# Performance work log

Hardware: AMD Instinct MI355X
Metric: run time of the kernel (lower is better)

## Reference

```python
import jax, jax.numpy as jnp
import numpy as np

B, T, C, H = 8, 2048, 1024, 64  # batch, seq (block_size), n_embd, head_size


def setup_inputs() -> dict:
    key = jax.random.key(0)
    kx, kq, kk, kv = jax.random.split(key, 4)
    s = 1.0 / np.sqrt(C)
    return {
        "x": jax.random.normal(kx, (B, T, C), dtype=jnp.float32),
        "Wq": jax.random.normal(kq, (C, H), dtype=jnp.float32) * s,
        "Wk": jax.random.normal(kk, (C, H), dtype=jnp.float32) * s,
        "Wv": jax.random.normal(kv, (C, H), dtype=jnp.float32) * s,
    }


def reference(x, Wq, Wk, Wv):
    t = x.shape[1]
    q = jnp.einsum("btc,ch->bth", x, Wq)
    k = jnp.einsum("btc,ch->bth", x, Wk)
    v = jnp.einsum("btc,ch->bth", x, Wv)
    scores = jnp.einsum("bqh,bkh->bqk", q, k) / jnp.sqrt(jnp.float32(H))
    causal = jnp.tril(jnp.ones((t, t), dtype=bool))  # tril mask
    scores = jnp.where(causal, scores, -jnp.inf)
    attn = jax.nn.softmax(scores, axis=-1)
    return jnp.einsum("bqk,bkh->bqh", attn, v)
```

## Files before the change

### kernel.cpp

```cpp
#include <hip/hip_runtime.h>
#include <hip/hip_bf16.h>

#define BB 8
#define TT 2048
#define CC 1024
#define HH 64
#define NSPLIT 8

typedef __attribute__((ext_vector_type(8)))  short bf16x8;
typedef __attribute__((ext_vector_type(4)))  float f32x4;
typedef __attribute__((ext_vector_type(16))) float f32x16;
typedef __attribute__((ext_vector_type(8)))  unsigned short us8;
typedef unsigned int u32;

static __device__ __forceinline__ unsigned short f2bf(float f) {
    union { float f; unsigned int u; } v; v.f = f;
    unsigned int u = v.u;
    return (unsigned short)((u + 0x7FFFu + ((u >> 16) & 1u)) >> 16);
}
static __device__ __forceinline__ float bf2f(unsigned short s) {
    union { u32 u; float f; } v; v.u = ((u32)s) << 16; return v.f;
}

__global__ __launch_bounds__(256) void prep_weights(
        const float* __restrict__ Wq, const float* __restrict__ Wk,
        const float* __restrict__ Wv, unsigned short* __restrict__ Wt) {
    __shared__ float tile[64][65];
    int w  = blockIdx.x >> 4;
    int c0 = (blockIdx.x & 15) * 64;
    const float* W = (w == 0) ? Wq : (w == 1) ? Wk : Wv;
    int li = threadIdx.x;
    {
        int c = li >> 2, h4 = (li & 3) * 16;
        const float* src = W + (size_t)(c0 + c) * HH + h4;
        #pragma unroll
        for (int i = 0; i < 4; ++i) {
            float4 v4 = *(const float4*)(src + i * 4);
            tile[c][h4 + i*4 + 0] = v4.x; tile[c][h4 + i*4 + 1] = v4.y;
            tile[c][h4 + i*4 + 2] = v4.z; tile[c][h4 + i*4 + 3] = v4.w;
        }
    }
    __syncthreads();
    float scale = (w == 0) ? 0.1803368802f : 1.0f;
    int h = li >> 2, cg = (li & 3) * 16;
    unsigned short* dst = Wt + (size_t)w * HH * CC + (size_t)h * CC + c0 + cg;
    #pragma unroll
    for (int i = 0; i < 16; ++i) dst[i] = f2bf(tile[cg + i][h] * scale);
}

__global__ __launch_bounds__(512, 4) void proj_qkv(
        const float* __restrict__ x, const unsigned short* __restrict__ Wt,
        unsigned short* __restrict__ Pp) {
    __shared__ unsigned short Xs[2][64 * 64];
    __shared__ unsigned short Ws[2][192 * 64];
    int tid = threadIdx.x;
    int wv = tid >> 6, lane = tid & 63;
    int quad = (lane >> 4) & 3, lq = lane & 15;
    int mg = wv >> 2, ng = wv & 3;
    int r0 = blockIdx.x * 64;
    int k0 = blockIdx.y * 512;

    int xr = tid >> 3, xg = tid & 7;
    const float* xsrc = x + (size_t)(r0 + xr) * CC + k0 + xg * 8;
    int xdst = xr * 64 + ((xg ^ (xr & 7)) * 8);
    float4 xa[2], xb[2];

    f32x4 acc[2][3];
    #pragma unroll
    for (int mt = 0; mt < 2; ++mt)
        #pragma unroll
        for (int nt = 0; nt < 3; ++nt)
            #pragma unroll
            for (int i = 0; i < 4; ++i) acc[mt][nt][i] = 0.0f;

    auto stageW = [&](int buf, int kc) {
        #pragma unroll
        for (int i = 0; i < 3; ++i) {
            int fp = tid + i * 512;
            int r = fp >> 3, pb = fp & 7, g = pb ^ (r & 7);
            const u32 __attribute__((address_space(1)))* gsrc =
                (const u32 __attribute__((address_space(1)))*)
                    (Wt + (size_t)r * CC + k0 + kc * 64 + g * 8);
            u32 __attribute__((address_space(3)))* ldst =
                (u32 __attribute__((address_space(3)))*)(&Ws[buf][fp * 8]);
            __builtin_amdgcn_global_load_lds(gsrc, ldst, 16, 0, 0);
        }
    };
    auto loadX = [&](int set, int kc) {
        xa[set] = *(const float4*)(xsrc + kc * 64);
        xb[set] = *(const float4*)(xsrc + kc * 64 + 4);
    };
    auto writeX = [&](int set, int buf) {
        unsigned short h[8];
        h[0]=f2bf(xa[set].x); h[1]=f2bf(xa[set].y);
        h[2]=f2bf(xa[set].z); h[3]=f2bf(xa[set].w);
        h[4]=f2bf(xb[set].x); h[5]=f2bf(xb[set].y);
        h[6]=f2bf(xb[set].z); h[7]=f2bf(xb[set].w);
        *(us8*)&Xs[buf][xdst] = *(const us8*)h;
    };

    loadX(0, 0); loadX(1, 1);
    stageW(0, 0);
    writeX(0, 0);

    for (int kc = 0; kc < 8; ++kc) {
        int cur = kc & 1;
        __syncthreads();
        if (kc < 7) stageW(1 - cur, kc + 1);
        if (kc < 6) loadX(kc & 1, kc + 2);
        #pragma unroll
        for (int ks = 0; ks < 2; ++ks) {
            int g = ks * 4 + quad;
            bf16x8 a[2], b[3];
            #pragma unroll
            for (int mt = 0; mt < 2; ++mt) {
                int arow = mg * 32 + mt * 16 + lq;
                a[mt] = *(const bf16x8*)&Xs[cur][arow * 64 + (g ^ (lq & 7)) * 8];
            }
            #pragma unroll
            for (int nt = 0; nt < 3; ++nt) {
                int brow = ng * 48 + nt * 16 + lq;
                b[nt] = *(const bf16x8*)&Ws[cur][brow * 64 + (g ^ (lq & 7)) * 8];
            }
            #pragma unroll
            for (int mt = 0; mt < 2; ++mt)
                #pragma unroll
                for (int nt = 0; nt < 3; ++nt)
                    acc[mt][nt] = __builtin_amdgcn_mfma_f32_16x16x32_bf16(
                        a[mt], b[nt], acc[mt][nt], 0, 0, 0);
        }
        if (kc < 7) writeX((kc + 1) & 1, 1 - cur);
    }

    unsigned short* Pb =
        Pp + ((size_t)blockIdx.y * (BB * TT) + r0) * 192;
    #pragma unroll
    for (int mt = 0; mt < 2; ++mt) {
        #pragma unroll
        for (int nt = 0; nt < 3; ++nt) {
            int g = ng * 48 + nt * 16 + lq;
            #pragma unroll
            for (int i = 0; i < 4; ++i) {
                int row = mg * 32 + mt * 16 + quad * 4 + i;
                Pb[(size_t)row * 192 + g] = f2bf(acc[mt][nt][i]);
            }
        }
    }
}

__global__ __launch_bounds__(256) void qkv_reduce(
        const unsigned short* __restrict__ Pp,
        unsigned short* __restrict__ qws, unsigned short* __restrict__ kws,
        unsigned short* __restrict__ vws) {
    __shared__ unsigned short Vt[64][72];
    int t = threadIdx.x;
    int br0 = blockIdx.x * 64;
    const size_t H2 = (size_t)BB * TT * 192;
    {
        int r = br0 + (t >> 2), cg = (t & 3) * 32;
        const unsigned short* p0 = Pp + (size_t)r * 192 + cg;
        const unsigned short* p1 = p0 + H2;
        unsigned short* dst = (cg < 64) ? (qws + (size_t)r * HH + cg)
                                        : (kws + (size_t)r * HH + (cg - 64));
        #pragma unroll
        for (int u = 0; u < 4; ++u) {
            us8 a = *(const us8*)(p0 + u * 8);
            us8 b = *(const us8*)(p1 + u * 8);
            unsigned short o[8];
            #pragma unroll
            for (int j = 0; j < 8; ++j) o[j] = f2bf(bf2f(a[j]) + bf2f(b[j]));
            *(us8*)(dst + u * 8) = *(const us8*)o;
        }
    }
    {
        int r = br0 + (t >> 2), ch = (t & 3) * 16;
        const unsigned short* p0 = Pp + (size_t)r * 192 + 128 + ch;
        const unsigned short* p1 = p0 + H2;
        #pragma unroll
        for (int u = 0; u < 2; ++u) {
            us8 a = *(const us8*)(p0 + u * 8);
            us8 b = *(const us8*)(p1 + u * 8);
            #pragma unroll
            for (int j = 0; j < 8; ++j)
                Vt[ch + u * 8 + j][r & 63] = f2bf(bf2f(a[j]) + bf2f(b[j]));
        }
    }
    __syncthreads();
    {
        int h = t >> 2, tb = (t & 3) * 16;
        int b = br0 >> 11, rr = br0 & (TT - 1);
        #pragma unroll
        for (int u = 0; u < 2; ++u)
            *(us8*)(vws + ((size_t)b * HH + h) * TT + rr + tb + u * 8) =
                *(const us8*)&Vt[h][tb + u * 8];
    }
}

__global__ __launch_bounds__(128, 3) void attn(
        const unsigned short* __restrict__ qws,
        const unsigned short* __restrict__ kws,
        const unsigned short* __restrict__ vws,
        unsigned short* __restrict__ Op, float* __restrict__ Lp) {
    __shared__ unsigned short Kt[32][72];
    __shared__ unsigned short Vt[64][40];
    __shared__ unsigned short Ps[64][40];
    int ti = blockIdx.x;
    int s  = blockIdx.y;
    int b  = blockIdx.z;
    int last = 2 * ti + 1;
    if (s > last) return;
    int tid = threadIdx.x, wv = tid >> 6, lane = tid & 63;
    int half = lane >> 5, l31 = lane & 31;

    bf16x8 qf[4];
    {
        const unsigned short* qp =
            qws + ((size_t)b * TT + ti * 64 + wv * 32 + l31) * HH + half * 8;
        #pragma unroll
        for (int ks = 0; ks < 4; ++ks) qf[ks] = *(const bf16x8*)(qp + ks * 16);
    }
    f32x16 O0, O1, Lc;
    #pragma unroll
    for (int i = 0; i < 16; ++i) { O0[i] = 0.f; O1[i] = 0.f; Lc[i] = 0.f; }
    bf16x8 ones;
    #pragma unroll
    for (int i = 0; i < 8; ++i) ones[i] = (short)0x3F80;

    int kr = tid >> 3, kg = tid & 7;
    int vh = tid >> 2, vkb = tid & 3;
    const unsigned short* ksrc0 = kws + ((size_t)b * TT + kr) * HH + kg * 8;
    const unsigned short* vsrc0 = vws + ((size_t)b * HH + vh) * TT + vkb * 8;

    us8 rk[2], rv[2];
    auto loadKV = [&](int jc) {
        rk[0] = *(const us8*)(ksrc0 + (size_t)(jc * 32) * HH);
        rk[1] = *(const us8*)(ksrc0 + (size_t)(jc * 32 + 16) * HH);
        rv[0] = *(const us8*)(vsrc0 + jc * 32);
        rv[1] = *(const us8*)(vsrc0 + (size_t)32 * TT + jc * 32);
    };
    auto writeKV = [&]() {
        *(us8*)&Kt[kr][kg * 8]       = rk[0];
        *(us8*)&Kt[kr + 16][kg * 8]  = rk[1];
        *(us8*)&Vt[vh][vkb * 8]      = rv[0];
        *(us8*)&Vt[vh + 32][vkb * 8] = rv[1];
    };

    loadKV(s);
    for (int jc = s; jc <= last; jc += NSPLIT) {
        __syncthreads();
        writeKV();
        if (jc + NSPLIT <= last) loadKV(jc + NSPLIT);
        __syncthreads();
        f32x16 S;
        #pragma unroll
        for (int i = 0; i < 16; ++i) S[i] = 0.f;
        #pragma unroll
        for (int ks = 0; ks < 4; ++ks) {
            bf16x8 kf = *(const bf16x8*)&Kt[l31][ks * 16 + half * 8];
            S = __builtin_amdgcn_mfma_f32_32x32x16_bf16(qf[ks], kf, S, 0, 0, 0);
        }
        bool diag = (jc >= 2 * ti + wv);
        #pragma unroll
        for (int r = 0; r < 16; ++r) {
            int pat = (r & 3) + 8 * (r >> 2) + 4 * half;
            float p = __builtin_amdgcn_exp2f(S[r]);
            if (diag && jc * 32 + l31 > ti * 64 + wv * 32 + pat) p = 0.0f;
            Ps[wv * 32 + pat][l31] = f2bf(p);
        }
        #pragma unroll
        for (int ks = 0; ks < 2; ++ks) {
            bf16x8 pa  = *(const bf16x8*)&Ps[wv * 32 + l31][ks * 16 + half * 8];
            bf16x8 vf0 = *(const bf16x8*)&Vt[l31][ks * 16 + half * 8];
            bf16x8 vf1 = *(const bf16x8*)&Vt[32 + l31][ks * 16 + half * 8];
            O0 = __builtin_amdgcn_mfma_f32_32x32x16_bf16(pa, vf0, O0, 0, 0, 0);
            O1 = __builtin_amdgcn_mfma_f32_32x32x16_bf16(pa, vf1, O1, 0, 0, 0);
            Lc = __builtin_amdgcn_mfma_f32_32x32x16_bf16(pa, ones, Lc, 0, 0, 0);
        }
    }
    unsigned short* Ob =
        Op + (((size_t)s * BB + b) * TT + ti * 64 + wv * 32) * HH;
    #pragma unroll
    for (int r = 0; r < 16; ++r) {
        int pat = (r & 3) + 8 * (r >> 2) + 4 * half;
        Ob[(size_t)pat * HH + l31]      = f2bf(O0[r]);
        Ob[(size_t)pat * HH + 32 + l31] = f2bf(O1[r]);
    }
    if (l31 == 0) {
        #pragma unroll
        for (int r = 0; r < 16; ++r) {
            int pat = (r & 3) + 8 * (r >> 2) + 4 * half;
            Lp[((size_t)s * BB + b) * TT + ti * 64 + wv * 32 + pat] = Lc[r];
        }
    }
}

__global__ __launch_bounds__(256) void norm_out(
        const unsigned short* __restrict__ Op, const float* __restrict__ Lp,
        float* __restrict__ out) {
    int idx = blockIdx.x * 256 + threadIdx.x;
    int g = idx >> 2;
    int hseg = (idx & 3) * 16;
    int ti = (g & (TT - 1)) >> 6;
    int ns = min(2 * ti + 2, NSPLIT);
    float a[16];
    #pragma unroll
    for (int j = 0; j < 16; ++j) a[j] = 0.f;
    float Ls = 0.f;
    for (int s = 0; s < ns; ++s) {
        const unsigned short* base =
            Op + ((size_t)s * BB * TT + g) * HH + hseg;
        us8 u0 = *(const us8*)base;
        us8 u1 = *(const us8*)(base + 8);
        #pragma unroll
        for (int j = 0; j < 8; ++j) { a[j] += bf2f(u0[j]); a[8 + j] += bf2f(u1[j]); }
        Ls += Lp[(size_t)s * BB * TT + g];
    }
    float inv = 1.0f / Ls;
    float* ob = out + (size_t)g * HH + hseg;
    #pragma unroll
    for (int q = 0; q < 4; ++q) {
        float4 v = make_float4(a[q*4] * inv, a[q*4+1] * inv,
                               a[q*4+2] * inv, a[q*4+3] * inv);
        ((float4*)ob)[q] = v;
    }
}

extern "C" void kernel_launch(void* const* d_in, const int* in_sizes, int n_in,
                              void* d_out, int out_size, void* d_ws, size_t ws_size,
                              hipStream_t stream) {
    (void)in_sizes; (void)n_in; (void)out_size; (void)ws_size;
    const float* x  = (const float*)d_in[0];
    const float* Wq = (const float*)d_in[1];
    const float* Wk = (const float*)d_in[2];
    const float* Wv = (const float*)d_in[3];
    float* out = (float*)d_out;

    char* ws = (char*)d_ws;
    unsigned short* Wt  = (unsigned short*)ws;
    unsigned short* qws = (unsigned short*)(ws + (1u << 19));
    unsigned short* kws = (unsigned short*)(ws + (1u << 19) + (1u << 21));
    unsigned short* vws = (unsigned short*)(ws + (1u << 19) + (2u << 21));
    unsigned short* Op  = (unsigned short*)(ws + (1u << 19) + (3u << 21));
    float*          Lp  = (float*)(ws + (1u << 19) + (3u << 21) + (1u << 24));
    unsigned short* Pp  = (unsigned short*)(ws + (1u << 19) + (3u << 21)
                                            + (1u << 24) + (1u << 19));

    prep_weights<<<48, 256, 0, stream>>>(Wq, Wk, Wv, Wt);
    proj_qkv<<<dim3(256, 2), 512, 0, stream>>>(x, Wt, Pp);
    qkv_reduce<<<256, 256, 0, stream>>>(Pp, qws, kws, vws);
    attn<<<dim3(32, NSPLIT, 8), 128, 0, stream>>>(qws, kws, vws, Op, Lp);
    norm_out<<<256, 256, 0, stream>>>(Op, Lp, out);
}
```

Baseline: 135.7 us.

## Drop split-K in QKV projection and fuse reduce into epilogue

The projection kernel now covers the full 1024-wide reduction per block instead of splitting K in two. The epilogue writes q, k and transposed v straight to their workspaces, so the partial buffer and the separate reduce kernel are removed. This saves a kernel launch and the round trip of partial sums through global memory, at the cost of half as many blocks, each with a loop twice as long.

```diff
diff --git a/kernel.cpp b/kernel.cpp
--- a/kernel.cpp
+++ b/kernel.cpp
@@ -11,6 +11,7 @@
 typedef __attribute__((ext_vector_type(4)))  float f32x4;
 typedef __attribute__((ext_vector_type(16))) float f32x16;
 typedef __attribute__((ext_vector_type(8)))  unsigned short us8;
+typedef __attribute__((ext_vector_type(4)))  unsigned short us4;
 typedef unsigned int u32;
 
 static __device__ __forceinline__ unsigned short f2bf(float f) {
@@ -50,7 +51,8 @@
 
 __global__ __launch_bounds__(512, 4) void proj_qkv(
         const float* __restrict__ x, const unsigned short* __restrict__ Wt,
-        unsigned short* __restrict__ Pp) {
+        unsigned short* __restrict__ qws, unsigned short* __restrict__ kws,
+        unsigned short* __restrict__ vws) {
     __shared__ unsigned short Xs[2][64 * 64];
     __shared__ unsigned short Ws[2][192 * 64];
     int tid = threadIdx.x;
@@ -58,10 +60,9 @@
     int quad = (lane >> 4) & 3, lq = lane & 15;
     int mg = wv >> 2, ng = wv & 3;
     int r0 = blockIdx.x * 64;
-    int k0 = blockIdx.y * 512;
 
     int xr = tid >> 3, xg = tid & 7;
-    const float* xsrc = x + (size_t)(r0 + xr) * CC + k0 + xg * 8;
+    const float* xsrc = x + (size_t)(r0 + xr) * CC + xg * 8;
     int xdst = xr * 64 + ((xg ^ (xr & 7)) * 8);
     float4 xa[2], xb[2];
 
@@ -80,7 +81,7 @@
             int r = fp >> 3, pb = fp & 7, g = pb ^ (r & 7);
             const u32 __attribute__((address_space(1)))* gsrc =
                 (const u32 __attribute__((address_space(1)))*)
-                    (Wt + (size_t)r * CC + k0 + kc * 64 + g * 8);
+                    (Wt + (size_t)r * CC + kc * 64 + g * 8);
             u32 __attribute__((address_space(3)))* ldst =
                 (u32 __attribute__((address_space(3)))*)(&Ws[buf][fp * 8]);
             __builtin_amdgcn_global_load_lds(gsrc, ldst, 16, 0, 0);
@@ -103,11 +104,11 @@
     stageW(0, 0);
     writeX(0, 0);
 
-    for (int kc = 0; kc < 8; ++kc) {
+    for (int kc = 0; kc < 16; ++kc) {
         int cur = kc & 1;
         __syncthreads();
-        if (kc < 7) stageW(1 - cur, kc + 1);
-        if (kc < 6) loadX(kc & 1, kc + 2);
+        if (kc < 15) stageW(1 - cur, kc + 1);
+        if (kc < 14) loadX(kc & 1, kc + 2);
         #pragma unroll
         for (int ks = 0; ks < 2; ++ks) {
             int g = ks * 4 + quad;
@@ -129,70 +130,35 @@
                     acc[mt][nt] = __builtin_amdgcn_mfma_f32_16x16x32_bf16(
                         a[mt], b[nt], acc[mt][nt], 0, 0, 0);
         }
-        if (kc < 7) writeX((kc + 1) & 1, 1 - cur);
-    }
-
-    unsigned short* Pb =
-        Pp + ((size_t)blockIdx.y * (BB * TT) + r0) * 192;
+        if (kc < 15) writeX((kc + 1) & 1, 1 - cur);
+    }
+
+    int bidx = r0 >> 11;
+    int t0base = r0 & (TT - 1);
     #pragma unroll
     for (int mt = 0; mt < 2; ++mt) {
         #pragma unroll
         for (int nt = 0; nt < 3; ++nt) {
-            int g = ng * 48 + nt * 16 + lq;
-            #pragma unroll
-            for (int i = 0; i < 4; ++i) {
-                int row = mg * 32 + mt * 16 + quad * 4 + i;
-                Pb[(size_t)row * 192 + g] = f2bf(acc[mt][nt][i]);
+            int gcol = ng * 48 + nt * 16 + lq;
+            int rloc = mg * 32 + mt * 16 + quad * 4;
+            if (gcol < 64) {
+                #pragma unroll
+                for (int i = 0; i < 4; ++i)
+                    qws[(size_t)(r0 + rloc + i) * HH + gcol] =
+                        f2bf(acc[mt][nt][i]);
+            } else if (gcol < 128) {
+                #pragma unroll
+                for (int i = 0; i < 4; ++i)
+                    kws[(size_t)(r0 + rloc + i) * HH + (gcol - 64)] =
+                        f2bf(acc[mt][nt][i]);
+            } else {
+                unsigned short o[4];
+                #pragma unroll
+                for (int i = 0; i < 4; ++i) o[i] = f2bf(acc[mt][nt][i]);
+                *(us4*)(vws + ((size_t)bidx * HH + (gcol - 128)) * TT
+                            + t0base + rloc) = *(const us4*)o;
             }
         }
-    }
-}
-
-__global__ __launch_bounds__(256) void qkv_reduce(
-        const unsigned short* __restrict__ Pp,
-        unsigned short* __restrict__ qws, unsigned short* __restrict__ kws,
-        unsigned short* __restrict__ vws) {
-    __shared__ unsigned short Vt[64][72];
-    int t = threadIdx.x;
-    int br0 = blockIdx.x * 64;
-    const size_t H2 = (size_t)BB * TT * 192;
-    {
-        int r = br0 + (t >> 2), cg = (t & 3) * 32;
-        const unsigned short* p0 = Pp + (size_t)r * 192 + cg;
-        const unsigned short* p1 = p0 + H2;
-        unsigned short* dst = (cg < 64) ? (qws + (size_t)r * HH + cg)
-                                        : (kws + (size_t)r * HH + (cg - 64));
-        #pragma unroll
-        for (int u = 0; u < 4; ++u) {
-            us8 a = *(const us8*)(p0 + u * 8);
-            us8 b = *(const us8*)(p1 + u * 8);
-            unsigned short o[8];
-            #pragma unroll
-            for (int j = 0; j < 8; ++j) o[j] = f2bf(bf2f(a[j]) + bf2f(b[j]));
-            *(us8*)(dst + u * 8) = *(const us8*)o;
-        }
-    }
-    {
-        int r = br0 + (t >> 2), ch = (t & 3) * 16;
-        const unsigned short* p0 = Pp + (size_t)r * 192 + 128 + ch;
-        const unsigned short* p1 = p0 + H2;
-        #pragma unroll
-        for (int u = 0; u < 2; ++u) {
-            us8 a = *(const us8*)(p0 + u * 8);
-            us8 b = *(const us8*)(p1 + u * 8);
-            #pragma unroll
-            for (int j = 0; j < 8; ++j)
-                Vt[ch + u * 8 + j][r & 63] = f2bf(bf2f(a[j]) + bf2f(b[j]));
-        }
-    }
-    __syncthreads();
-    {
-        int h = t >> 2, tb = (t & 3) * 16;
-        int b = br0 >> 11, rr = br0 & (TT - 1);
-        #pragma unroll
-        for (int u = 0; u < 2; ++u)
-            *(us8*)(vws + ((size_t)b * HH + h) * TT + rr + tb + u * 8) =
-                *(const us8*)&Vt[h][tb + u * 8];
     }
 }
 
@@ -342,12 +308,9 @@
     unsigned short* vws = (unsigned short*)(ws + (1u << 19) + (2u << 21));
     unsigned short* Op  = (unsigned short*)(ws + (1u << 19) + (3u << 21));
     float*          Lp  = (float*)(ws + (1u << 19) + (3u << 21) + (1u << 24));
-    unsigned short* Pp  = (unsigned short*)(ws + (1u << 19) + (3u << 21)
-                                            + (1u << 24) + (1u << 19));
 
     prep_weights<<<48, 256, 0, stream>>>(Wq, Wk, Wv, Wt);
-    proj_qkv<<<dim3(256, 2), 512, 0, stream>>>(x, Wt, Pp);
-    qkv_reduce<<<256, 256, 0, stream>>>(Pp, qws, kws, vws);
+    proj_qkv<<<256, 512, 0, stream>>>(x, Wt, qws, kws, vws);
     attn<<<dim3(32, NSPLIT, 8), 128, 0, stream>>>(qws, kws, vws, Op, Lp);
     norm_out<<<256, 256, 0, stream>>>(Op, Lp, out);
 }
```

Result: no change. 136.3 us (+0.5%).
